# Performance work log

Measured on AMD Instinct MI355X. Metric: run time of the kernel, lower is better.

Reference implementation:

```python
import jax, jax.numpy as jnp
import numpy as np

L, B, S, D, H, F, V = 12, 2, 1024, 768, 12, 3072, 50257
DK = D // H
EPS = 1e-6


def _ln(x, a, b):
    # torch: a*(x-mean)/(std+eps)+b with unbiased std (ddof=1)
    m = x.mean(-1, keepdims=True)
    std = jnp.sqrt(((x - m) ** 2).sum(-1, keepdims=True) / (x.shape[-1] - 1))
    return a * (x - m) / (std + EPS) + b


def _pos_encoding(s, d):
    pos = jnp.arange(s, dtype=jnp.float32)[:, None]
    div = jnp.exp(jnp.arange(0, d, 2, dtype=jnp.float32) * (-np.log(10000.0) / d))
    pe = jnp.zeros((s, d), dtype=jnp.float32)
    pe = pe.at[:, 0::2].set(jnp.sin(pos * div))
    pe = pe.at[:, 1::2].set(jnp.cos(pos * div))
    return pe


def setup_inputs() -> dict:
    key = jax.random.key(0)
    ks = jax.random.split(key, 8)
    n = lambda k, sh: 0.02 * jax.random.normal(k, sh, dtype=jnp.float32)
    return dict(
        emb=n(ks[0], (V, D)),
        Wq=n(ks[1], (L, D, D)),
        Wk=n(ks[2], (L, D, D)),
        Wv=n(ks[3], (L, D, D)),
        Wo=n(ks[4], (L, D, D)),
        ln1_a=jnp.ones((L, D), jnp.float32),
        ln1_b=jnp.zeros((L, D), jnp.float32),
        ln2_a=jnp.ones((L, D), jnp.float32),
        ln2_b=jnp.zeros((L, D), jnp.float32),
        W1=n(ks[5], (L, D, F)),
        b1=jnp.zeros((L, F), jnp.float32),
        W2=n(ks[6], (L, F, D)),
        b2=jnp.zeros((L, D), jnp.float32),
        fn_a=jnp.ones((D,), jnp.float32),
        fn_b=jnp.zeros((D,), jnp.float32),
        pb=jnp.zeros((V,), jnp.float32),
        x=jax.random.randint(ks[7], (B, S), 0, V, dtype=jnp.int32),
    )


def reference(emb, Wq, Wk, Wv, Wo, ln1_a, ln1_b, ln2_a, ln2_b, W1, b1, W2, b2, fn_a, fn_b, pb, x):
    b, s = x.shape
    d = emb.shape[1]
    h = emb[x] * jnp.sqrt(jnp.float32(d)) + _pos_encoding(s, d)  # [B,S,D]
    causal = jnp.tril(jnp.ones((s, s), dtype=bool))

    def block(hh, p):
        wq, wk, wv, wo, a1, bb1n, a2, bb2n, w1, fb1, w2, fb2 = p
        xn = _ln(hh, a1, bb1n)
        q = (xn @ wq).reshape(b, s, H, DK)
        k = (xn @ wk).reshape(b, s, H, DK)
        v = (xn @ wv).reshape(b, s, H, DK)
        scores = jnp.einsum('bqhd,bkhd->bhqk', q, k) / jnp.sqrt(jnp.float32(DK))
        scores = jnp.where(causal, scores, -1e9)  # masked_fill_(mask==0, -1e9)
        attn = jax.nn.softmax(scores, axis=-1)
        o = jnp.einsum('bhqk,bkhd->bqhd', attn, v).reshape(b, s, d)
        hh = hh + o @ wo
        xn2 = _ln(hh, a2, bb2n)
        hh = hh + (jax.nn.relu(xn2 @ w1 + fb1) @ w2 + fb2)
        return hh, None

    h, _ = jax.lax.scan(block, h, (Wq, Wk, Wv, Wo, ln1_a, ln1_b, ln2_a, ln2_b, W1, b1, W2, b2))
    h = _ln(h, fn_a, fn_b)
    logits = h @ emb.T + pb  # tied-weight projection
    return logits
```

## Files before the change

### kernel.cpp

```cpp
#include <hip/hip_runtime.h>
#include <math.h>

constexpr int Lc = 12, Bc = 2, Sc = 1024, Dc = 768, Hc = 12, Fc = 3072, Vc = 50257, DKc = 64;
constexpr int Tc = Bc * Sc;
constexpr int QKVN = 3 * Dc;
constexpr int Vpad = 50304;

typedef __attribute__((ext_vector_type(8))) __bf16 bf16x8;
typedef __attribute__((ext_vector_type(8))) unsigned short u16x8;
typedef __attribute__((ext_vector_type(4))) float f32x4;

__device__ __forceinline__ unsigned short f2b(float f) {
  union { float f; unsigned int u; } v; v.f = f;
  unsigned int r = v.u + 0x7FFFu + ((v.u >> 16) & 1u);
  return (unsigned short)(r >> 16);
}
__device__ __forceinline__ float b2f(unsigned short u) {
  return __uint_as_float(((unsigned int)u) << 16);
}

__device__ __forceinline__ void gload16(const void* g, void* l) {
  __builtin_amdgcn_global_load_lds((const __attribute__((address_space(1))) void*)g,
                                   (__attribute__((address_space(3))) void*)l, 16, 0, 0);
}

__device__ __forceinline__ float bred_sum(float v, volatile float* sb) {
#pragma unroll
  for (int o = 32; o; o >>= 1) v += __shfl_down(v, o);
  int w = threadIdx.x >> 6;
  __syncthreads();
  if ((threadIdx.x & 63) == 0) sb[w] = v;
  __syncthreads();
  return sb[0] + sb[1] + sb[2] + sb[3];
}

__global__ __launch_bounds__(256) void embed_kernel(const float* __restrict__ emb,
                                                    const int* __restrict__ x,
                                                    float* __restrict__ h) {
  int t = blockIdx.x;
  int s = t & (Sc - 1);
  int tok = x[t];
  const float scale = 27.712812921102035f;
  for (int d = threadIdx.x; d < Dc; d += 256) {
    int i = d >> 1;
    float div = __expf((float)(2 * i) * (-9.210340371976184f / (float)Dc));
    float ang = (float)s * div;
    float pe = (d & 1) ? cosf(ang) : sinf(ang);
    h[(size_t)t * Dc + d] = emb[(size_t)tok * Dc + d] * scale + pe;
  }
}

__global__ __launch_bounds__(256) void convert_emb_kernel(const float* __restrict__ emb,
                                                          ushort* __restrict__ embT) {
  const size_t total4 = (size_t)Vpad * Dc / 4;
  for (size_t i = (size_t)blockIdx.x * 256 + threadIdx.x; i < total4; i += (size_t)gridDim.x * 256) {
    size_t e = i * 4;
    int row = (int)(e / Dc);
    ushort4 w;
    if (row < Vc) {
      float4 f = *(const float4*)&emb[e];
      w.x = f2b(f.x); w.y = f2b(f.y); w.z = f2b(f.z); w.w = f2b(f.w);
    } else {
      w = make_ushort4(0, 0, 0, 0);
    }
    *(ushort4*)&embT[e] = w;
  }
}

__global__ __launch_bounds__(256) void transpose_layer_kernel(
    const float* __restrict__ Wq, const float* __restrict__ Wk, const float* __restrict__ Wv,
    const float* __restrict__ Wo, const float* __restrict__ W1, const float* __restrict__ W2,
    int l, ushort* __restrict__ WqkvT, ushort* __restrict__ WoT,
    ushort* __restrict__ W1T, ushort* __restrict__ W2T) {
  __shared__ float tile[64][65];
  int bid = blockIdx.x;
  const float* src; ushort* dst; int N, Kd, tt;
  if (bid < 432) {
    int m = bid / 144; tt = bid % 144;
    src = (m == 0 ? Wq : (m == 1 ? Wk : Wv)) + (size_t)l * Dc * Dc;
    N = Dc; Kd = Dc; dst = WqkvT + (size_t)m * Dc * Dc;
  } else if (bid < 576) {
    tt = bid - 432; src = Wo + (size_t)l * Dc * Dc; N = Dc; Kd = Dc; dst = WoT;
  } else if (bid < 1152) {
    tt = bid - 576; src = W1 + (size_t)l * Dc * Fc; N = Fc; Kd = Dc; dst = W1T;
  } else {
    tt = bid - 1152; src = W2 + (size_t)l * Fc * Dc; N = Dc; Kd = Fc; dst = W2T;
  }
  int nt = N / 64;
  int k0 = (tt / nt) * 64, n0 = (tt % nt) * 64;
  int t = threadIdx.x;
  int r0 = t >> 4, c4 = (t & 15) * 4;
#pragma unroll
  for (int rr = 0; rr < 4; ++rr) {
    int r = r0 + rr * 16;
    float4 f = *(const float4*)&src[(size_t)(k0 + r) * N + n0 + c4];
    tile[r][c4] = f.x; tile[r][c4 + 1] = f.y; tile[r][c4 + 2] = f.z; tile[r][c4 + 3] = f.w;
  }
  __syncthreads();
  int i0 = t >> 4, j4 = (t & 15) * 4;
#pragma unroll
  for (int rr = 0; rr < 4; ++rr) {
    int i = i0 + rr * 16;
    ushort4 w;
    w.x = f2b(tile[j4][i]); w.y = f2b(tile[j4 + 1][i]);
    w.z = f2b(tile[j4 + 2][i]); w.w = f2b(tile[j4 + 3][i]);
    *(ushort4*)&dst[(size_t)(n0 + i) * Kd + k0 + j4] = w;
  }
}

__global__ __launch_bounds__(256) void ln_kernel(const float* __restrict__ in,
                                                 const float* __restrict__ ga,
                                                 const float* __restrict__ be,
                                                 ushort* __restrict__ out) {
  __shared__ float sb[4];
  int t = blockIdx.x;
  const float* row = in + (size_t)t * Dc;
  int tid = threadIdx.x;
  float x0 = row[tid], x1 = row[tid + 256], x2 = row[tid + 512];
  float s = bred_sum(x0 + x1 + x2, sb);
  float mean = s * (1.0f / 768.0f);
  float d0 = x0 - mean, d1 = x1 - mean, d2 = x2 - mean;
  float vs = bred_sum(d0 * d0 + d1 * d1 + d2 * d2, sb);
  float inv = 1.0f / (sqrtf(vs * (1.0f / 767.0f)) + 1e-6f);
  ushort* orow = out + (size_t)t * Dc;
  orow[tid] = f2b(ga[tid] * d0 * inv + be[tid]);
  orow[tid + 256] = f2b(ga[tid + 256] * d1 * inv + be[tid + 256]);
  orow[tid + 512] = f2b(ga[tid + 512] * d2 * inv + be[tid + 512]);
}

template <typename OT, bool BIAS, bool RELU, bool RESID>
__global__ __launch_bounds__(256) void gemm_bf16(const ushort* __restrict__ A,
                                                 const ushort* __restrict__ Bt,
                                                 const float* __restrict__ bias,
                                                 const float* __restrict__ resid,
                                                 OT* __restrict__ C,
                                                 int M, int N, int K, int ldc) {
  __shared__ __attribute__((aligned(16))) ushort sm[8192];
  ushort* As = sm;
  ushort* Bs = sm + 4096;
  const int tid = threadIdx.x;
  const int wid = tid >> 6, lane = tid & 63;
  const int wr = wid >> 1, wc = wid & 1;
  const int kg = lane >> 4, fr = lane & 15;
  const int bm = blockIdx.y * 128, bn = blockIdx.x * 128;

  f32x4 acc[4][4] = {};

  for (int k0 = 0; k0 < K; k0 += 32) {
    const ushort* Ab = A + (size_t)bm * K + k0;
    const ushort* Bb = Bt + (size_t)bn * K + k0;
#pragma unroll
    for (int it = 0; it < 2; ++it) {
      int c = it * 256 + tid;
      int row = c >> 2, kc = (c & 3) * 8;
      gload16(Ab + (size_t)row * K + kc, &As[(it * 256 + wid * 64) * 8]);
    }
#pragma unroll
    for (int it = 0; it < 2; ++it) {
      int c = it * 256 + tid;
      int row = c >> 2, kc = (c & 3) * 8;
      gload16(Bb + (size_t)row * K + kc, &Bs[(it * 256 + wid * 64) * 8]);
    }
    __syncthreads();

    bf16x8 af[4], bfr[4];
#pragma unroll
    for (int i = 0; i < 4; ++i)
      af[i] = *(const bf16x8*)&As[(wr * 64 + i * 16 + fr) * 32 + kg * 8];
#pragma unroll
    for (int j = 0; j < 4; ++j)
      bfr[j] = *(const bf16x8*)&Bs[(wc * 64 + j * 16 + fr) * 32 + kg * 8];
#pragma unroll
    for (int i = 0; i < 4; ++i)
#pragma unroll
      for (int j = 0; j < 4; ++j)
        acc[i][j] = __builtin_amdgcn_mfma_f32_16x16x32_bf16(af[i], bfr[j], acc[i][j], 0, 0, 0);
    __syncthreads();
  }

  const int r0 = kg * 4;
#pragma unroll
  for (int i = 0; i < 4; ++i) {
    int mbase = bm + wr * 64 + i * 16 + r0;
#pragma unroll
    for (int j = 0; j < 4; ++j) {
      int n = bn + wc * 64 + j * 16 + fr;
      if (n < N) {
        float bv = BIAS ? bias[n] : 0.0f;
#pragma unroll
        for (int r = 0; r < 4; ++r) {
          float v = acc[i][j][r] + bv;
          if (RELU) v = fmaxf(v, 0.0f);
          size_t idx = (size_t)(mbase + r) * ldc + n;
          if (RESID) v += resid[idx];
          if constexpr (sizeof(OT) == 2) C[idx] = (OT)f2b(v);
          else C[idx] = (OT)v;
        }
      }
    }
  }
}

__global__ __launch_bounds__(256) void flash_attn_kernel(const ushort* __restrict__ qkv,
                                                         ushort* __restrict__ o) {
  const int qt = blockIdx.x;
  const int hb = blockIdx.y;
  const int hh = hb % Hc, b = hb / Hc;
  const int tid = threadIdx.x;
  const int w = tid >> 6, lane = tid & 63;
  const int g = lane >> 4, c = lane & 15;

  __shared__ __attribute__((aligned(16))) ushort Ks[64 * 64];
  __shared__ __attribute__((aligned(16))) ushort Vt[64 * 64];
  __shared__ __attribute__((aligned(16))) ushort Ps[4][16 * 64];

  const int q0 = qt * 64;
  const int qw = q0 + w * 16;

  bf16x8 aq[2];
  {
    const size_t qrow = (size_t)(b * Sc + qw + c) * QKVN + hh * DKc;
#pragma unroll
    for (int kk = 0; kk < 2; ++kk)
      aq[kk] = *(const bf16x8*)&qkv[qrow + kk * 32 + g * 8];
  }

  float m_r[4], l_r[4];
  f32x4 oa[4] = {};
#pragma unroll
  for (int r = 0; r < 4; ++r) { m_r[r] = -1e30f; l_r[r] = 0.f; }

  const int ntiles = qt + 1;
  for (int t = 0; t < ntiles; ++t) {
    const int kv0 = t * 64;
#pragma unroll
    for (int it = 0; it < 2; ++it) {
      int idx = it * 256 + tid;
      int kv = idx >> 3, ck = idx & 7;
      u16x8 kd = *(const u16x8*)&qkv[(size_t)(b * Sc + kv0 + kv) * QKVN + Dc + hh * DKc + ck * 8];
      *(u16x8*)((char*)Ks + ((kv * 128 + ck * 16) ^ ((kv & 7) << 4))) = kd;
    }
    {
      int kv = tid >> 2;
      int dbase = (tid & 3) * 16;
      const ushort* vrow = &qkv[(size_t)(b * Sc + kv0 + kv) * QKVN + 2 * Dc + hh * DKc + dbase];
      u16x8 v0 = *(const u16x8*)&vrow[0];
      u16x8 v1 = *(const u16x8*)&vrow[8];
#pragma unroll
      for (int dd = 0; dd < 8; ++dd) {
        int d0 = dbase + dd, d1 = dbase + 8 + dd;
        *(ushort*)((char*)Vt + ((d0 * 128 + kv * 2) ^ ((d0 & 7) << 4))) = v0[dd];
        *(ushort*)((char*)Vt + ((d1 * 128 + kv * 2) ^ ((d1 & 7) << 4))) = v1[dd];
      }
    }
    __syncthreads();

    f32x4 sacc[4] = {};
#pragma unroll
    for (int jn = 0; jn < 4; ++jn) {
      int kvl = jn * 16 + c;
#pragma unroll
      for (int kk = 0; kk < 2; ++kk) {
        bf16x8 bk = *(const bf16x8*)((char*)Ks + ((kvl * 128 + kk * 64 + g * 16) ^ ((kvl & 7) << 4)));
        sacc[jn] = __builtin_amdgcn_mfma_f32_16x16x32_bf16(aq[kk], bk, sacc[jn], 0, 0, 0);
      }
    }

    const bool last = (t == ntiles - 1);
    float p[4][4];
#pragma unroll
    for (int jn = 0; jn < 4; ++jn) {
      int kvg = kv0 + jn * 16 + c;
#pragma unroll
      for (int r = 0; r < 4; ++r) {
        float s = sacc[jn][r] * 0.125f;
        if (last && kvg > qw + g * 4 + r) s = -1e30f;
        p[jn][r] = s;
      }
    }
#pragma unroll
    for (int r = 0; r < 4; ++r) {
      float mx = fmaxf(fmaxf(p[0][r], p[1][r]), fmaxf(p[2][r], p[3][r]));
#pragma unroll
      for (int off = 1; off < 16; off <<= 1) mx = fmaxf(mx, __shfl_xor(mx, off));
      float mnew = fmaxf(m_r[r], mx);
      float sf = __expf(m_r[r] - mnew);
      m_r[r] = mnew;
      float rs = 0.f;
#pragma unroll
      for (int jn = 0; jn < 4; ++jn) {
        float e = __expf(p[jn][r] - mnew);
        p[jn][r] = e;
        rs += e;
      }
#pragma unroll
      for (int off = 1; off < 16; off <<= 1) rs += __shfl_xor(rs, off);
      l_r[r] = l_r[r] * sf + rs;
#pragma unroll
      for (int jd = 0; jd < 4; ++jd) oa[jd][r] *= sf;
    }

    {
      ushort* pw = Ps[w];
#pragma unroll
      for (int jn = 0; jn < 4; ++jn)
#pragma unroll
        for (int r = 0; r < 4; ++r) {
          int row = g * 4 + r, col = jn * 16 + c;
          *(ushort*)((char*)pw + ((row * 128 + col * 2) ^ ((row & 7) << 4))) = f2b(p[jn][r]);
        }
      bf16x8 ap[2];
#pragma unroll
      for (int kk = 0; kk < 2; ++kk)
        ap[kk] = *(const bf16x8*)((char*)pw + ((c * 128 + kk * 64 + g * 16) ^ ((c & 7) << 4)));
#pragma unroll
      for (int jd = 0; jd < 4; ++jd) {
        int d = jd * 16 + c;
#pragma unroll
        for (int kk = 0; kk < 2; ++kk) {
          bf16x8 bv = *(const bf16x8*)((char*)Vt + ((d * 128 + kk * 64 + g * 16) ^ ((d & 7) << 4)));
          oa[jd] = __builtin_amdgcn_mfma_f32_16x16x32_bf16(ap[kk], bv, oa[jd], 0, 0, 0);
        }
      }
    }
    __syncthreads();
  }

#pragma unroll
  for (int r = 0; r < 4; ++r) {
    int q = qw + g * 4 + r;
    float inv = 1.0f / l_r[r];
    size_t base = (size_t)(b * Sc + q) * Dc + hh * DKc;
#pragma unroll
    for (int jd = 0; jd < 4; ++jd)
      o[base + jd * 16 + c] = f2b(oa[jd][r] * inv);
  }
}

extern "C" void kernel_launch(void* const* d_in, const int* in_sizes, int n_in,
                              void* d_out, int out_size, void* d_ws, size_t ws_size,
                              hipStream_t stream) {
  const float* emb  = (const float*)d_in[0];
  const float* Wq   = (const float*)d_in[1];
  const float* Wk   = (const float*)d_in[2];
  const float* Wv   = (const float*)d_in[3];
  const float* Wo   = (const float*)d_in[4];
  const float* ln1a = (const float*)d_in[5];
  const float* ln1b = (const float*)d_in[6];
  const float* ln2a = (const float*)d_in[7];
  const float* ln2b = (const float*)d_in[8];
  const float* W1   = (const float*)d_in[9];
  const float* b1   = (const float*)d_in[10];
  const float* W2   = (const float*)d_in[11];
  const float* b2   = (const float*)d_in[12];
  const float* fna  = (const float*)d_in[13];
  const float* fnb  = (const float*)d_in[14];
  const float* pb   = (const float*)d_in[15];
  const int*   x    = (const int*)d_in[16];
  float* out = (float*)d_out;

  float* h = (float*)d_ws;
  ushort* xn    = (ushort*)(h + (size_t)Tc * Dc);
  ushort* qkv   = xn + (size_t)Tc * Dc;
  ushort* ao    = qkv + (size_t)Tc * QKVN;
  ushort* f1    = ao + (size_t)Tc * Dc;
  ushort* embT  = f1 + (size_t)Tc * Fc;
  ushort* WqkvT = embT + (size_t)Vpad * Dc;
  ushort* WoT   = WqkvT + (size_t)QKVN * Dc;
  ushort* W1T   = WoT + (size_t)Dc * Dc;
  ushort* W2T   = W1T + (size_t)Fc * Dc;

  embed_kernel<<<Tc, 256, 0, stream>>>(emb, x, h);
  convert_emb_kernel<<<2048, 256, 0, stream>>>(emb, embT);

  dim3 gQKV(QKVN / 128, Tc / 128);
  dim3 gD(Dc / 128, Tc / 128);
  dim3 gF(Fc / 128, Tc / 128);
  dim3 gA(Sc / 64, Bc * Hc);
  for (int l = 0; l < Lc; ++l) {
    transpose_layer_kernel<<<1728, 256, 0, stream>>>(Wq, Wk, Wv, Wo, W1, W2, l,
                                                     WqkvT, WoT, W1T, W2T);
    ln_kernel<<<Tc, 256, 0, stream>>>(h, ln1a + l * Dc, ln1b + l * Dc, xn);
    gemm_bf16<ushort, false, false, false><<<gQKV, 256, 0, stream>>>(
        xn, WqkvT, nullptr, nullptr, qkv, Tc, QKVN, Dc, QKVN);
    flash_attn_kernel<<<gA, 256, 0, stream>>>(qkv, ao);
    gemm_bf16<float, false, false, true><<<gD, 256, 0, stream>>>(
        ao, WoT, nullptr, h, h, Tc, Dc, Dc, Dc);
    ln_kernel<<<Tc, 256, 0, stream>>>(h, ln2a + l * Dc, ln2b + l * Dc, xn);
    gemm_bf16<ushort, true, true, false><<<gF, 256, 0, stream>>>(
        xn, W1T, b1 + (size_t)l * Fc, nullptr, f1, Tc, Fc, Dc, Fc);
    gemm_bf16<float, true, false, true><<<gD, 256, 0, stream>>>(
        f1, W2T, b2 + (size_t)l * Dc, h, h, Tc, Dc, Fc, Dc);
  }
  ln_kernel<<<Tc, 256, 0, stream>>>(h, fna, fnb, xn);
  dim3 gL(Vpad / 128, Tc / 128);
  gemm_bf16<float, true, false, false><<<gL, 256, 0, stream>>>(
      xn, embT, pb, nullptr, out, Tc, Vc, Dc, Vc);
}
```

Before: 3.379 ms.

## Use 64-row GEMM tiles for narrow outputs, swap logits grid, reverse attention tiles

Templates the GEMM on the M tile height, so the two D-wide GEMMs (Wo and W2) use 64x128 tiles. This doubles their block count from 96 to 192 and fills more compute units. The logits GEMM swaps its grid axes so neighbouring blocks share the same embedding tile for better L2 reuse. Flash attention now schedules the most expensive causal query tiles first to reduce the tail. Smaller tiles lower per-block data reuse and MFMA density.

Result: faster. 3.010 ms (-10.9%).

```diff
diff --git a/kernel.cpp b/kernel.cpp
--- a/kernel.cpp
+++ b/kernel.cpp
@@ -128,29 +128,35 @@
   orow[tid + 512] = f2b(ga[tid + 512] * d2 * inv + be[tid + 512]);
 }
 
-template <typename OT, bool BIAS, bool RELU, bool RESID>
+template <typename OT, int BM, bool BIAS, bool RELU, bool RESID, bool SWAP>
 __global__ __launch_bounds__(256) void gemm_bf16(const ushort* __restrict__ A,
                                                  const ushort* __restrict__ Bt,
                                                  const float* __restrict__ bias,
                                                  const float* __restrict__ resid,
                                                  OT* __restrict__ C,
                                                  int M, int N, int K, int ldc) {
-  __shared__ __attribute__((aligned(16))) ushort sm[8192];
+  constexpr int MW = BM / 64;
+  constexpr int NW = 4 / MW;
+  constexpr int WCOLS = 128 / NW;
+  constexpr int NJ = WCOLS / 16;
+  __shared__ __attribute__((aligned(16))) ushort sm[(BM + 128) * 32];
   ushort* As = sm;
-  ushort* Bs = sm + 4096;
+  ushort* Bs = sm + BM * 32;
   const int tid = threadIdx.x;
   const int wid = tid >> 6, lane = tid & 63;
-  const int wr = wid >> 1, wc = wid & 1;
+  const int wr = (MW == 2) ? (wid >> 1) : 0;
+  const int wc = (MW == 2) ? (wid & 1) : wid;
   const int kg = lane >> 4, fr = lane & 15;
-  const int bm = blockIdx.y * 128, bn = blockIdx.x * 128;
-
-  f32x4 acc[4][4] = {};
+  const int bm = (SWAP ? blockIdx.x : blockIdx.y) * BM;
+  const int bn = (SWAP ? blockIdx.y : blockIdx.x) * 128;
+
+  f32x4 acc[4][NJ] = {};
 
   for (int k0 = 0; k0 < K; k0 += 32) {
     const ushort* Ab = A + (size_t)bm * K + k0;
     const ushort* Bb = Bt + (size_t)bn * K + k0;
 #pragma unroll
-    for (int it = 0; it < 2; ++it) {
+    for (int it = 0; it < BM / 64; ++it) {
       int c = it * 256 + tid;
       int row = c >> 2, kc = (c & 3) * 8;
       gload16(Ab + (size_t)row * K + kc, &As[(it * 256 + wid * 64) * 8]);
@@ -163,17 +169,17 @@
     }
     __syncthreads();
 
-    bf16x8 af[4], bfr[4];
+    bf16x8 af[4], bfr[NJ];
 #pragma unroll
     for (int i = 0; i < 4; ++i)
       af[i] = *(const bf16x8*)&As[(wr * 64 + i * 16 + fr) * 32 + kg * 8];
 #pragma unroll
-    for (int j = 0; j < 4; ++j)
-      bfr[j] = *(const bf16x8*)&Bs[(wc * 64 + j * 16 + fr) * 32 + kg * 8];
+    for (int j = 0; j < NJ; ++j)
+      bfr[j] = *(const bf16x8*)&Bs[(wc * WCOLS + j * 16 + fr) * 32 + kg * 8];
 #pragma unroll
     for (int i = 0; i < 4; ++i)
 #pragma unroll
-      for (int j = 0; j < 4; ++j)
+      for (int j = 0; j < NJ; ++j)
         acc[i][j] = __builtin_amdgcn_mfma_f32_16x16x32_bf16(af[i], bfr[j], acc[i][j], 0, 0, 0);
     __syncthreads();
   }
@@ -183,8 +189,8 @@
   for (int i = 0; i < 4; ++i) {
     int mbase = bm + wr * 64 + i * 16 + r0;
 #pragma unroll
-    for (int j = 0; j < 4; ++j) {
-      int n = bn + wc * 64 + j * 16 + fr;
+    for (int j = 0; j < NJ; ++j) {
+      int n = bn + wc * WCOLS + j * 16 + fr;
       if (n < N) {
         float bv = BIAS ? bias[n] : 0.0f;
 #pragma unroll
@@ -203,7 +209,7 @@
 
 __global__ __launch_bounds__(256) void flash_attn_kernel(const ushort* __restrict__ qkv,
                                                          ushort* __restrict__ o) {
-  const int qt = blockIdx.x;
+  const int qt = gridDim.x - 1 - blockIdx.x;
   const int hb = blockIdx.y;
   const int hh = hb % Hc, b = hb / Hc;
   const int tid = threadIdx.x;
@@ -374,26 +380,26 @@
   convert_emb_kernel<<<2048, 256, 0, stream>>>(emb, embT);
 
   dim3 gQKV(QKVN / 128, Tc / 128);
-  dim3 gD(Dc / 128, Tc / 128);
+  dim3 gD64(Dc / 128, Tc / 64);
   dim3 gF(Fc / 128, Tc / 128);
   dim3 gA(Sc / 64, Bc * Hc);
   for (int l = 0; l < Lc; ++l) {
     transpose_layer_kernel<<<1728, 256, 0, stream>>>(Wq, Wk, Wv, Wo, W1, W2, l,
                                                      WqkvT, WoT, W1T, W2T);
     ln_kernel<<<Tc, 256, 0, stream>>>(h, ln1a + l * Dc, ln1b + l * Dc, xn);
-    gemm_bf16<ushort, false, false, false><<<gQKV, 256, 0, stream>>>(
+    gemm_bf16<ushort, 128, false, false, false, false><<<gQKV, 256, 0, stream>>>(
         xn, WqkvT, nullptr, nullptr, qkv, Tc, QKVN, Dc, QKVN);
     flash_attn_kernel<<<gA, 256, 0, stream>>>(qkv, ao);
-    gemm_bf16<float, false, false, true><<<gD, 256, 0, stream>>>(
+    gemm_bf16<float, 64, false, false, true, false><<<gD64, 256, 0, stream>>>(
         ao, WoT, nullptr, h, h, Tc, Dc, Dc, Dc);
     ln_kernel<<<Tc, 256, 0, stream>>>(h, ln2a + l * Dc, ln2b + l * Dc, xn);
-    gemm_bf16<ushort, true, true, false><<<gF, 256, 0, stream>>>(
+    gemm_bf16<ushort, 128, true, true, false, false><<<gF, 256, 0, stream>>>(
         xn, W1T, b1 + (size_t)l * Fc, nullptr, f1, Tc, Fc, Dc, Fc);
-    gemm_bf16<float, true, false, true><<<gD, 256, 0, stream>>>(
+    gemm_bf16<float, 64, true, false, true, false><<<gD64, 256, 0, stream>>>(
         f1, W2T, b2 + (size_t)l * Dc, h, h, Tc, Dc, Fc, Dc);
   }
   ln_kernel<<<Tc, 256, 0, stream>>>(h, fna, fnb, xn);
-  dim3 gL(Vpad / 128, Tc / 128);
-  gemm_bf16<float, true, false, false><<<gL, 256, 0, stream>>>(
+  dim3 gL(Tc / 128, Vpad / 128);
+  gemm_bf16<float, 128, true, false, false, true><<<gL, 256, 0, stream>>>(
       xn, embT, pb, nullptr, out, Tc, Vc, Dc, Vc);
 }
```
